# Optimization experiments

Hardware: AMD Instinct MI355X
Metric: run time of the kernel (lower is better)

## Reference

```python
import jax, jax.numpy as jnp
import numpy as np

D = 128
HIDDEN = 512
N = 2048


def setup_inputs() -> dict:
    key = jax.random.key(0)
    k_x, k0, k1, k2 = jax.random.split(key, 4)
    x = jax.random.normal(k_x, (N, D), dtype=jnp.float32)
    # LocallyConnected init: uniform(-sqrt(1/in), sqrt(1/in))
    b0 = 1.0 / np.sqrt(D)
    b1 = 1.0 / np.sqrt(HIDDEN)
    W0 = jax.random.uniform(k0, (D, D, HIDDEN), jnp.float32, -b0, b0)
    W1 = jax.random.uniform(k1, (D, HIDDEN, HIDDEN), jnp.float32, -b1, b1)
    W2 = jax.random.uniform(k2, (D, HIDDEN, 1), jnp.float32, -b1, b1)
    return {"x": x, "W0": W0, "W1": W1, "W2": W2}


def reference(x, W0, W1, W2):
    n, d = x.shape
    # masking layer: matmul with diag(mask[i]) == elementwise zero-out of diagonal
    mask = 1.0 - jnp.eye(d, dtype=x.dtype)          # [d, d]
    h = x[:, None, :] * mask[None, :, :]            # [n, d, d]
    # per-node locally-connected MLP
    h = jax.nn.leaky_relu(jnp.einsum('ndi,dio->ndo', h, W0))   # [n, d, hidden]
    h = jax.nn.leaky_relu(jnp.einsum('ndi,dio->ndo', h, W1))   # [n, d, hidden]
    h = jnp.einsum('ndi,dio->ndo', h, W2)                      # [n, d, 1]
    return h.squeeze(-1)                                       # [n, d]
```

## Files before the change

### kernel.cpp

```cpp
#include <hip/hip_runtime.h>

#define DD 128
#define HH 512
#define NN 2048
#define NT 64
#define PLD 516

typedef __bf16 bf16x8 __attribute__((ext_vector_type(8)));
typedef __bf16 bf16x4 __attribute__((ext_vector_type(4)));
typedef float  floatx4 __attribute__((ext_vector_type(4)));

__global__ void cvt_x(const float* __restrict__ x, __bf16* __restrict__ xb) {
    int t = blockIdx.x * blockDim.x + threadIdx.x;
    float4 v = *(const float4*)(x + (size_t)t * 4);
    bf16x4 o;
    o[0] = (__bf16)v.x; o[1] = (__bf16)v.y; o[2] = (__bf16)v.z; o[3] = (__bf16)v.w;
    *(bf16x4*)(xb + (size_t)t * 4) = o;
}

__global__ void pack_w(const float* __restrict__ W, __bf16* __restrict__ Wp, int nks) {
    __shared__ __bf16 Ls[32 * PLD];
    const int d  = blockIdx.x / nks;
    const int ks = blockIdx.x % nks;
    const int tid = threadIdx.x;
    const float* src = W + ((size_t)(d * nks + ks) * 32) * HH;

#pragma unroll
    for (int it = 0; it < 16; ++it) {
        int e = (it * 256 + tid) * 4;
        float4 v = *(const float4*)(src + e);
        bf16x4 o;
        o[0] = (__bf16)v.x; o[1] = (__bf16)v.y; o[2] = (__bf16)v.z; o[3] = (__bf16)v.w;
        *(bf16x4*)(Ls + (e >> 9) * PLD + (e & 511)) = o;
    }
    __syncthreads();

#pragma unroll
    for (int it = 0; it < 8; ++it) {
        int ch = it * 256 + tid;
        int c  = ch & 15;
        int q  = (ch >> 4) & 3;
        int ct = ch >> 6;
        bf16x8 v;
#pragma unroll
        for (int j = 0; j < 8; ++j)
            v[j] = Ls[(q * 8 + j) * PLD + ct * 16 + c];
        *(bf16x8*)(Wp + ((size_t)(d * 32 + ct) * nks + ks) * 512 + (ch & 63) * 8) = v;
    }
}

__launch_bounds__(512, 4)
__global__ void grandag_main(const __bf16* __restrict__ xb,
                             const __bf16* __restrict__ W0p,
                             const __bf16* __restrict__ W1p,
                             const float* __restrict__ W2,
                             float* __restrict__ out) {
    __shared__ __bf16 h1s[NT * HH];
    __shared__ float  outp[NT];

    const int b  = blockIdx.x;
    const int d  = ((b >> 8) << 3) | (b & 7);
    const int n0 = ((b >> 3) & 31) * NT;

    const int tid = threadIdx.x;
    const int w   = tid >> 6;
    const int l   = tid & 63;
    const int lc  = l & 15;
    const int lq  = l >> 4;
    const int sw  = lc & 7;
    const int lane16 = lq * 16 + lc;

    const int ksz = d >> 5;
    const int lqz = (d >> 3) & 3;
    const int jz  = d & 7;

    if (tid < NT) outp[tid] = 0.f;

    {
        floatx4 acc[4][4] = {};
        const __bf16* W0b = W0p + ((size_t)(d * 32 + w * 4) * 4) * 512 + (size_t)lane16 * 8;
        const __bf16* xbb = xb + (size_t)(n0 + lc) * DD + lq * 8;
#pragma unroll
        for (int ks = 0; ks < 4; ks++) {
            bf16x8 wf[4];
#pragma unroll
            for (int mt = 0; mt < 4; mt++)
                wf[mt] = *(const bf16x8*)(W0b + (size_t)(mt * 4 + ks) * 512);
            const bool domask = (ks == ksz) && (lq == lqz);
#pragma unroll
            for (int nt = 0; nt < 4; nt++) {
                bf16x8 xf = *(const bf16x8*)(xbb + (size_t)(16 * nt) * DD + ks * 32);
                if (domask) {
#pragma unroll
                    for (int j = 0; j < 8; j++)
                        if (j == jz) xf[j] = (__bf16)0.f;
                }
#pragma unroll
                for (int mt = 0; mt < 4; mt++)
                    acc[mt][nt] = __builtin_amdgcn_mfma_f32_16x16x32_bf16(
                        wf[mt], xf, acc[mt][nt], 0, 0, 0);
            }
        }
#pragma unroll
        for (int mt = 0; mt < 4; mt++) {
            const int chunk = 8 * w + 2 * mt + (lq >> 1);
#pragma unroll
            for (int nt = 0; nt < 4; nt++) {
                bf16x4 o;
#pragma unroll
                for (int g = 0; g < 4; g++) {
                    float v = acc[mt][nt][g];
                    o[g] = (__bf16)fmaxf(v, 0.01f * v);
                }
                *(bf16x4*)(h1s + (16 * nt + lc) * HH + ((chunk ^ sw) << 3) + ((lq & 1) << 2)) = o;
            }
        }
    }
    __syncthreads();

    floatx4 acc2[4][4] = {};
    {
        const __bf16* W1b = W1p + ((size_t)(d * 32 + w * 4) * 16) * 512 + (size_t)lane16 * 8;
        const __bf16* h1b = h1s + lc * HH;
#pragma unroll
        for (int ks = 0; ks < 16; ks++) {
            bf16x8 wf[4];
#pragma unroll
            for (int mt = 0; mt < 4; mt++)
                wf[mt] = *(const bf16x8*)(W1b + (size_t)(mt * 16 + ks) * 512);
            const int hoff = ((4 * ks + lq) ^ sw) << 3;
#pragma unroll
            for (int nt = 0; nt < 4; nt++) {
                bf16x8 hf = *(const bf16x8*)(h1b + 16 * nt * HH + hoff);
#pragma unroll
                for (int mt = 0; mt < 4; mt++)
                    acc2[mt][nt] = __builtin_amdgcn_mfma_f32_16x16x32_bf16(
                        wf[mt], hf, acc2[mt][nt], 0, 0, 0);
            }
        }
    }

    {
        const float* W2b = W2 + (size_t)d * HH + w * 64 + lq * 4;
#pragma unroll
        for (int nt = 0; nt < 4; nt++) {
            float s = 0.f;
#pragma unroll
            for (int mt = 0; mt < 4; mt++) {
                floatx4 w2q = *(const floatx4*)(W2b + mt * 16);
#pragma unroll
                for (int g = 0; g < 4; g++) {
                    float v = acc2[mt][nt][g];
                    s += fmaxf(v, 0.01f * v) * w2q[g];
                }
            }
            s += __shfl_xor(s, 16, 64);
            s += __shfl_xor(s, 32, 64);
            if (l < 16) atomicAdd(&outp[16 * nt + lc], s);
        }
    }
    __syncthreads();
    if (tid < NT) out[(size_t)(n0 + tid) * DD + d] = outp[tid];
}

extern "C" void kernel_launch(void* const* d_in, const int* in_sizes, int n_in,
                              void* d_out, int out_size, void* d_ws, size_t ws_size,
                              hipStream_t stream) {
    const float* x  = (const float*)d_in[0];
    const float* W0 = (const float*)d_in[1];
    const float* W1 = (const float*)d_in[2];
    const float* W2 = (const float*)d_in[3];
    float* out = (float*)d_out;

    __bf16* W0p = (__bf16*)d_ws;
    __bf16* W1p = (__bf16*)((char*)d_ws + (size_t)DD * DD * HH * 2);
    __bf16* xb  = (__bf16*)((char*)d_ws + (size_t)DD * DD * HH * 2
                                        + (size_t)DD * HH * HH * 2);

    cvt_x<<<dim3(NN * DD / (256 * 4)), 256, 0, stream>>>(x, xb);
    pack_w<<<dim3(DD * (DD / 32)), 256, 0, stream>>>(W0, W0p, DD / 32);
    pack_w<<<dim3(DD * (HH / 32)), 256, 0, stream>>>(W1, W1p, HH / 32);

    grandag_main<<<dim3(DD * (NN / NT)), 512, 0, stream>>>(xb, W0p, W1p, W2, out);
}
```

Measured before the change: 404.8 us.

## Switch main GEMMs to 32x32x16 MFMA with repacked weights and prefetch

Changes both layer GEMMs from 16x16x32 to 32x32x16 bf16 MFMA tiles, repacking W0/W1 into a matching 32-wide fragment layout and changing the h1 shared-memory indexing. Weight fragments are software-prefetched one k-step ahead to overlap global loads with MFMA work. The final reduction replaces LDS atomics with per-wave partial buffers summed by 64 threads. The larger tiles reduce fragment loads per FLOP, at the cost of different register pressure and LDS access patterns.

```diff
diff --git a/kernel.cpp b/kernel.cpp
--- a/kernel.cpp
+++ b/kernel.cpp
@@ -8,7 +8,8 @@
 
 typedef __bf16 bf16x8 __attribute__((ext_vector_type(8)));
 typedef __bf16 bf16x4 __attribute__((ext_vector_type(4)));
-typedef float  floatx4 __attribute__((ext_vector_type(4)));
+typedef float  floatx4  __attribute__((ext_vector_type(4)));
+typedef float  floatx16 __attribute__((ext_vector_type(16)));
 
 __global__ void cvt_x(const float* __restrict__ x, __bf16* __restrict__ xb) {
     int t = blockIdx.x * blockDim.x + threadIdx.x;
@@ -18,12 +19,13 @@
     *(bf16x4*)(xb + (size_t)t * 4) = o;
 }
 
-__global__ void pack_w(const float* __restrict__ W, __bf16* __restrict__ Wp, int nks) {
+__global__ void pack_w(const float* __restrict__ W, __bf16* __restrict__ Wp, int nks32) {
     __shared__ __bf16 Ls[32 * PLD];
-    const int d  = blockIdx.x / nks;
-    const int ks = blockIdx.x % nks;
+    const int d  = blockIdx.x / nks32;
+    const int ks = blockIdx.x % nks32;
     const int tid = threadIdx.x;
-    const float* src = W + ((size_t)(d * nks + ks) * 32) * HH;
+    const int nks16 = nks32 * 2;
+    const float* src = W + ((size_t)(d * nks32 + ks) * 32) * HH;
 
 #pragma unroll
     for (int it = 0; it < 16; ++it) {
@@ -37,15 +39,16 @@
 
 #pragma unroll
     for (int it = 0; it < 8; ++it) {
-        int ch = it * 256 + tid;
-        int c  = ch & 15;
-        int q  = (ch >> 4) & 3;
-        int ct = ch >> 6;
+        int u  = it * 256 + tid;
+        int l  = u & 63;
+        int ct = (u >> 6) & 15;
+        int kh = u >> 10;
+        int lr = l & 31, lh = l >> 5;
         bf16x8 v;
 #pragma unroll
         for (int j = 0; j < 8; ++j)
-            v[j] = Ls[(q * 8 + j) * PLD + ct * 16 + c];
-        *(bf16x8*)(Wp + ((size_t)(d * 32 + ct) * nks + ks) * 512 + (ch & 63) * 8) = v;
+            v[j] = Ls[(kh * 16 + lh * 8 + j) * PLD + ct * 32 + lr];
+        *(bf16x8*)(Wp + ((size_t)(d * 16 + ct) * nks16 + (ks * 2 + kh)) * 512 + l * 8) = v;
     }
 }
 
@@ -56,7 +59,7 @@
                              const float* __restrict__ W2,
                              float* __restrict__ out) {
     __shared__ __bf16 h1s[NT * HH];
-    __shared__ float  outp[NT];
+    __shared__ float  outp2[8][NT];
 
     const int b  = blockIdx.x;
     const int d  = ((b >> 8) << 3) | (b & 7);
@@ -65,102 +68,128 @@
     const int tid = threadIdx.x;
     const int w   = tid >> 6;
     const int l   = tid & 63;
-    const int lc  = l & 15;
-    const int lq  = l >> 4;
-    const int sw  = lc & 7;
-    const int lane16 = lq * 16 + lc;
-
-    const int ksz = d >> 5;
-    const int lqz = (d >> 3) & 3;
+    const int lr  = l & 31;
+    const int lh  = l >> 5;
+    const int swz = lr & 7;
+
+    const int kz  = d >> 4;
+    const int lhz = (d >> 3) & 1;
     const int jz  = d & 7;
 
-    if (tid < NT) outp[tid] = 0.f;
-
     {
-        floatx4 acc[4][4] = {};
-        const __bf16* W0b = W0p + ((size_t)(d * 32 + w * 4) * 4) * 512 + (size_t)lane16 * 8;
-        const __bf16* xbb = xb + (size_t)(n0 + lc) * DD + lq * 8;
-#pragma unroll
-        for (int ks = 0; ks < 4; ks++) {
-            bf16x8 wf[4];
-#pragma unroll
-            for (int mt = 0; mt < 4; mt++)
-                wf[mt] = *(const bf16x8*)(W0b + (size_t)(mt * 4 + ks) * 512);
-            const bool domask = (ks == ksz) && (lq == lqz);
-#pragma unroll
-            for (int nt = 0; nt < 4; nt++) {
-                bf16x8 xf = *(const bf16x8*)(xbb + (size_t)(16 * nt) * DD + ks * 32);
-                if (domask) {
-#pragma unroll
-                    for (int j = 0; j < 8; j++)
-                        if (j == jz) xf[j] = (__bf16)0.f;
+        floatx16 acc[2][2] = {};
+        const __bf16* W0b = W0p + ((size_t)(d * 16 + w * 2) * 8) * 512 + (size_t)l * 8;
+        const __bf16* xbb = xb + (size_t)(n0 + lr) * DD + lh * 8;
+
+        bf16x8 wa0 = *(const bf16x8*)(W0b);
+        bf16x8 wa1 = *(const bf16x8*)(W0b + (size_t)8 * 512);
+#pragma unroll
+        for (int ks = 0; ks < 8; ks += 2) {
+            bf16x8 wb0 = *(const bf16x8*)(W0b + (size_t)(ks + 1) * 512);
+            bf16x8 wb1 = *(const bf16x8*)(W0b + (size_t)(8 + ks + 1) * 512);
+            bf16x8 x0 = *(const bf16x8*)(xbb + (size_t)ks * 16);
+            bf16x8 x1 = *(const bf16x8*)(xbb + (size_t)32 * DD + ks * 16);
+            if (ks == kz && lh == lhz) {
+#pragma unroll
+                for (int j = 0; j < 8; j++)
+                    if (j == jz) { x0[j] = (__bf16)0.f; x1[j] = (__bf16)0.f; }
+            }
+            acc[0][0] = __builtin_amdgcn_mfma_f32_32x32x16_bf16(wa0, x0, acc[0][0], 0, 0, 0);
+            acc[0][1] = __builtin_amdgcn_mfma_f32_32x32x16_bf16(wa0, x1, acc[0][1], 0, 0, 0);
+            acc[1][0] = __builtin_amdgcn_mfma_f32_32x32x16_bf16(wa1, x0, acc[1][0], 0, 0, 0);
+            acc[1][1] = __builtin_amdgcn_mfma_f32_32x32x16_bf16(wa1, x1, acc[1][1], 0, 0, 0);
+            wa0 = *(const bf16x8*)(W0b + (size_t)((ks + 2) & 7) * 512);
+            wa1 = *(const bf16x8*)(W0b + (size_t)(8 + ((ks + 2) & 7)) * 512);
+            x0 = *(const bf16x8*)(xbb + (size_t)(ks + 1) * 16);
+            x1 = *(const bf16x8*)(xbb + (size_t)32 * DD + (ks + 1) * 16);
+            if (ks + 1 == kz && lh == lhz) {
+#pragma unroll
+                for (int j = 0; j < 8; j++)
+                    if (j == jz) { x0[j] = (__bf16)0.f; x1[j] = (__bf16)0.f; }
+            }
+            acc[0][0] = __builtin_amdgcn_mfma_f32_32x32x16_bf16(wb0, x0, acc[0][0], 0, 0, 0);
+            acc[0][1] = __builtin_amdgcn_mfma_f32_32x32x16_bf16(wb0, x1, acc[0][1], 0, 0, 0);
+            acc[1][0] = __builtin_amdgcn_mfma_f32_32x32x16_bf16(wb1, x0, acc[1][0], 0, 0, 0);
+            acc[1][1] = __builtin_amdgcn_mfma_f32_32x32x16_bf16(wb1, x1, acc[1][1], 0, 0, 0);
+        }
+#pragma unroll
+        for (int mt = 0; mt < 2; mt++) {
+#pragma unroll
+            for (int q2 = 0; q2 < 4; q2++) {
+                const int chunk = 8 * w + 4 * mt + q2;
+#pragma unroll
+                for (int nt = 0; nt < 2; nt++) {
+                    const int row = nt * 32 + lr;
+                    bf16x4 o;
+#pragma unroll
+                    for (int i = 0; i < 4; i++) {
+                        float v = acc[mt][nt][q2 * 4 + i];
+                        o[i] = (__bf16)fmaxf(v, 0.01f * v);
+                    }
+                    *(bf16x4*)(h1s + (size_t)row * HH + ((chunk ^ swz) << 3) + 4 * lh) = o;
                 }
-#pragma unroll
-                for (int mt = 0; mt < 4; mt++)
-                    acc[mt][nt] = __builtin_amdgcn_mfma_f32_16x16x32_bf16(
-                        wf[mt], xf, acc[mt][nt], 0, 0, 0);
-            }
-        }
-#pragma unroll
-        for (int mt = 0; mt < 4; mt++) {
-            const int chunk = 8 * w + 2 * mt + (lq >> 1);
-#pragma unroll
-            for (int nt = 0; nt < 4; nt++) {
-                bf16x4 o;
-#pragma unroll
-                for (int g = 0; g < 4; g++) {
-                    float v = acc[mt][nt][g];
-                    o[g] = (__bf16)fmaxf(v, 0.01f * v);
+            }
+        }
+    }
+    __syncthreads();
+
+    floatx16 acc2[2][2] = {};
+    {
+        const __bf16* W1b  = W1p + ((size_t)(d * 16 + w * 2) * 32) * 512 + (size_t)l * 8;
+        const __bf16* h1b0 = h1s + (size_t)lr * HH;
+        const __bf16* h1b1 = h1s + (size_t)(32 + lr) * HH;
+
+        bf16x8 wa0 = *(const bf16x8*)(W1b);
+        bf16x8 wa1 = *(const bf16x8*)(W1b + (size_t)32 * 512);
+#pragma unroll
+        for (int ks = 0; ks < 32; ks += 2) {
+            bf16x8 wb0 = *(const bf16x8*)(W1b + (size_t)(ks + 1) * 512);
+            bf16x8 wb1 = *(const bf16x8*)(W1b + (size_t)(32 + ks + 1) * 512);
+            bf16x8 h0  = *(const bf16x8*)(h1b0 + (((2 * ks + lh) ^ swz) << 3));
+            bf16x8 h1v = *(const bf16x8*)(h1b1 + (((2 * ks + lh) ^ swz) << 3));
+            acc2[0][0] = __builtin_amdgcn_mfma_f32_32x32x16_bf16(wa0, h0,  acc2[0][0], 0, 0, 0);
+            acc2[0][1] = __builtin_amdgcn_mfma_f32_32x32x16_bf16(wa0, h1v, acc2[0][1], 0, 0, 0);
+            acc2[1][0] = __builtin_amdgcn_mfma_f32_32x32x16_bf16(wa1, h0,  acc2[1][0], 0, 0, 0);
+            acc2[1][1] = __builtin_amdgcn_mfma_f32_32x32x16_bf16(wa1, h1v, acc2[1][1], 0, 0, 0);
+            wa0 = *(const bf16x8*)(W1b + (size_t)((ks + 2) & 31) * 512);
+            wa1 = *(const bf16x8*)(W1b + (size_t)(32 + ((ks + 2) & 31)) * 512);
+            h0  = *(const bf16x8*)(h1b0 + (((2 * (ks + 1) + lh) ^ swz) << 3));
+            h1v = *(const bf16x8*)(h1b1 + (((2 * (ks + 1) + lh) ^ swz) << 3));
+            acc2[0][0] = __builtin_amdgcn_mfma_f32_32x32x16_bf16(wb0, h0,  acc2[0][0], 0, 0, 0);
+            acc2[0][1] = __builtin_amdgcn_mfma_f32_32x32x16_bf16(wb0, h1v, acc2[0][1], 0, 0, 0);
+            acc2[1][0] = __builtin_amdgcn_mfma_f32_32x32x16_bf16(wb1, h0,  acc2[1][0], 0, 0, 0);
+            acc2[1][1] = __builtin_amdgcn_mfma_f32_32x32x16_bf16(wb1, h1v, acc2[1][1], 0, 0, 0);
+        }
+    }
+
+    {
+        const float* W2b = W2 + (size_t)d * HH + w * 64 + lh * 4;
+#pragma unroll
+        for (int nt = 0; nt < 2; nt++) {
+            float s = 0.f;
+#pragma unroll
+            for (int mt = 0; mt < 2; mt++) {
+#pragma unroll
+                for (int q2 = 0; q2 < 4; q2++) {
+                    floatx4 w2q = *(const floatx4*)(W2b + mt * 32 + 8 * q2);
+#pragma unroll
+                    for (int i = 0; i < 4; i++) {
+                        float v = acc2[mt][nt][q2 * 4 + i];
+                        s += fmaxf(v, 0.01f * v) * w2q[i];
+                    }
                 }
-                *(bf16x4*)(h1s + (16 * nt + lc) * HH + ((chunk ^ sw) << 3) + ((lq & 1) << 2)) = o;
-            }
+            }
+            s += __shfl_xor(s, 32, 64);
+            if (!lh) outp2[w][nt * 32 + lr] = s;
         }
     }
     __syncthreads();
-
-    floatx4 acc2[4][4] = {};
-    {
-        const __bf16* W1b = W1p + ((size_t)(d * 32 + w * 4) * 16) * 512 + (size_t)lane16 * 8;
-        const __bf16* h1b = h1s + lc * HH;
-#pragma unroll
-        for (int ks = 0; ks < 16; ks++) {
-            bf16x8 wf[4];
-#pragma unroll
-            for (int mt = 0; mt < 4; mt++)
-                wf[mt] = *(const bf16x8*)(W1b + (size_t)(mt * 16 + ks) * 512);
-            const int hoff = ((4 * ks + lq) ^ sw) << 3;
-#pragma unroll
-            for (int nt = 0; nt < 4; nt++) {
-                bf16x8 hf = *(const bf16x8*)(h1b + 16 * nt * HH + hoff);
-#pragma unroll
-                for (int mt = 0; mt < 4; mt++)
-                    acc2[mt][nt] = __builtin_amdgcn_mfma_f32_16x16x32_bf16(
-                        wf[mt], hf, acc2[mt][nt], 0, 0, 0);
-            }
-        }
-    }
-
-    {
-        const float* W2b = W2 + (size_t)d * HH + w * 64 + lq * 4;
-#pragma unroll
-        for (int nt = 0; nt < 4; nt++) {
-            float s = 0.f;
-#pragma unroll
-            for (int mt = 0; mt < 4; mt++) {
-                floatx4 w2q = *(const floatx4*)(W2b + mt * 16);
-#pragma unroll
-                for (int g = 0; g < 4; g++) {
-                    float v = acc2[mt][nt][g];
-                    s += fmaxf(v, 0.01f * v) * w2q[g];
-                }
-            }
-            s += __shfl_xor(s, 16, 64);
-            s += __shfl_xor(s, 32, 64);
-            if (l < 16) atomicAdd(&outp[16 * nt + lc], s);
-        }
-    }
-    __syncthreads();
-    if (tid < NT) out[(size_t)(n0 + tid) * DD + d] = outp[tid];
+    if (tid < NT) {
+        float v = 0.f;
+#pragma unroll
+        for (int ww = 0; ww < 8; ww++) v += outp2[ww][tid];
+        out[(size_t)(n0 + tid) * DD + d] = v;
+    }
 }
 
 extern "C" void kernel_launch(void* const* d_in, const int* in_sizes, int n_in,
```

New measurement: 418.9 us. 1.03x slower.
